# Kernel optimization log

Measured on AMD Instinct MI355X. Metric: run time of the kernel, lower is better.

The kernel has to match this reference:

```python
import jax, jax.numpy as jnp
import numpy as np

N_LAYER = 3
N_HEAD = 12
D_K = 64
D_V = 64
D_MODEL = 768
D_INNER = 4096
LN_EPS = 1e-5
BN_EPS = 1e-5
PAD_ID = 1


def _layernorm(x, g, b):
    m = jnp.mean(x, axis=-1, keepdims=True)
    v = jnp.mean((x - m) ** 2, axis=-1, keepdims=True)
    return g * (x - m) / jnp.sqrt(v + LN_EPS) + b


def _batchnorm(x, g, b):
    # training-mode BatchNorm1d: per-feature batch statistics
    m = jnp.mean(x, axis=0)
    v = jnp.mean((x - m) ** 2, axis=0)
    return g * (x - m) / jnp.sqrt(v + BN_EPS) + b


def setup_inputs() -> dict:
    key = jax.random.key(0)
    ks = jax.random.split(key, 24)
    B, C, S, H = 4, 4, 256, D_MODEL
    inp = {
        'input_ids': jax.random.randint(ks[0], (B, C, S), 0, 50000, dtype=jnp.int64) if jax.config.read('jax_enable_x64') else jax.random.randint(ks[0], (B, C, S), 0, 50000, dtype=jnp.int32),
        'roberta_attn': jax.random.normal(ks[1], (B, C, S, H), dtype=jnp.float32),
        'pooled_output': jax.random.normal(ks[2], (B * C, H), dtype=jnp.float32),
        'commonsense_mask': jax.random.uniform(ks[3], (B, C, S, S), dtype=jnp.float32),
        'dependency_mask': jax.random.uniform(ks[4], (B, C, S, S), dtype=jnp.float32),
        'entity_mask': jax.random.uniform(ks[5], (B, C, S), dtype=jnp.float32),
        'sentiment_mask': jax.random.uniform(ks[6], (B, C, S, S), dtype=jnp.float32),
    }
    s = 0.02
    inp['lin_w'] = s * jax.random.normal(ks[7], (H, N_LAYER * 4), dtype=jnp.float32)
    inp['lin_b'] = jnp.zeros((N_LAYER * 4,), jnp.float32)
    inp['Wq'] = s * jax.random.normal(ks[8], (N_LAYER, H, N_HEAD * D_K), dtype=jnp.float32)
    inp['bq'] = jnp.zeros((N_LAYER, N_HEAD * D_K), jnp.float32)
    inp['Wk'] = s * jax.random.normal(ks[9], (N_LAYER, H, N_HEAD * D_K), dtype=jnp.float32)
    inp['bk'] = jnp.zeros((N_LAYER, N_HEAD * D_K), jnp.float32)
    inp['Wv'] = s * jax.random.normal(ks[10], (N_LAYER, H, N_HEAD * D_V), dtype=jnp.float32)
    inp['bv'] = jnp.zeros((N_LAYER, N_HEAD * D_V), jnp.float32)
    inp['Wo'] = s * jax.random.normal(ks[11], (N_LAYER, N_HEAD * D_V, H), dtype=jnp.float32)
    inp['bo'] = jnp.zeros((N_LAYER, H), jnp.float32)
    inp['ln1_g'] = jnp.ones((N_LAYER, H), jnp.float32)
    inp['ln1_b'] = jnp.zeros((N_LAYER, H), jnp.float32)
    inp['W1'] = s * jax.random.normal(ks[12], (N_LAYER, H, D_INNER), dtype=jnp.float32)
    inp['b1'] = jnp.zeros((N_LAYER, D_INNER), jnp.float32)
    inp['W2'] = s * jax.random.normal(ks[13], (N_LAYER, D_INNER, H), dtype=jnp.float32)
    inp['b2'] = jnp.zeros((N_LAYER, H), jnp.float32)
    inp['ln2_g'] = jnp.ones((N_LAYER, H), jnp.float32)
    inp['ln2_b'] = jnp.zeros((N_LAYER, H), jnp.float32)
    inp['bnt_g'] = jnp.ones((H,), jnp.float32)
    inp['bnt_b'] = jnp.zeros((H,), jnp.float32)
    inp['pool_w'] = s * jax.random.normal(ks[14], (H, H), dtype=jnp.float32)
    inp['pool_b'] = jnp.zeros((H,), jnp.float32)
    inp['bn_g'] = jnp.ones((H,), jnp.float32)
    inp['bn_b'] = jnp.zeros((H,), jnp.float32)
    inp['cls_w'] = s * jax.random.normal(ks[15], (H, 1), dtype=jnp.float32)
    inp['cls_b'] = jnp.zeros((1,), jnp.float32)
    return inp


def reference(input_ids, roberta_attn, pooled_output, commonsense_mask, dependency_mask,
              entity_mask, sentiment_mask, lin_w, lin_b, Wq, bq, Wk, bk, Wv, bv, Wo, bo,
              ln1_g, ln1_b, W1, b1, W2, b2, ln2_g, ln2_b, bnt_g, bnt_b,
              pool_w, pool_b, bn_g, bn_b, cls_w, cls_b):
    B, C, S = input_ids.shape
    H = roberta_attn.shape[-1]
    N = B * C
    x = roberta_attn.reshape(N, S, H)

    # learned softmax fusion weights over the 4 relational masks, per layer
    w = jnp.mean(x, axis=1) @ lin_w + lin_b                       # [N, 3*4]
    w = jax.nn.softmax(w.reshape(N, N_LAYER, 4).transpose(1, 0, 2), axis=-1)  # [3, N, 4]

    ent = jnp.broadcast_to(entity_mask[:, :, None, :], (B, C, S, S))
    masks = jnp.stack([
        commonsense_mask.reshape(N, S, S),
        dependency_mask.reshape(N, S, S),
        ent.reshape(N, S, S),
        sentiment_mask.reshape(N, S, S),
    ], axis=1)                                                     # [N, 4, S, S]
    bias = jnp.einsum('lnm,nmqk->lnqk', w, masks)                  # [3, N, S, S]

    non_pad = (input_ids.reshape(N, S) != PAD_ID).astype(x.dtype)[:, :, None]  # [N, S, 1]

    enc = x
    scale = 1.0 / np.sqrt(D_K).astype(np.float32)
    for l in range(N_LAYER):
        residual = enc
        q = (enc @ Wq[l] + bq[l]).reshape(N, S, N_HEAD, D_K)
        k = (enc @ Wk[l] + bk[l]).reshape(N, S, N_HEAD, D_K)
        v = (enc @ Wv[l] + bv[l]).reshape(N, S, N_HEAD, D_V)
        scores = jnp.einsum('nqhd,nkhd->nhqk', q, k) * scale + bias[l][:, None]  # [N,H,S,S]
        attn = jax.nn.softmax(scores, axis=-1)
        o = jnp.einsum('nhqk,nkhd->nqhd', attn, v).reshape(N, S, N_HEAD * D_V)
        o = o @ Wo[l] + bo[l]
        enc = _layernorm(o + residual, ln1_g[l], ln1_b[l]) * non_pad
        residual = enc
        f = jax.nn.relu(enc @ W1[l] + b1[l]) @ W2[l] + b2[l]
        enc = _layernorm(f + residual, ln2_g[l], ln2_b[l]) * non_pad

    enc = _batchnorm(enc.reshape(N * S, H), bnt_g, bnt_b).reshape(N, S, H)
    seq = x + enc
    pooled = jnp.tanh(seq[:, 0] @ pool_w + pool_b)
    pooled = _batchnorm(pooled, bn_g, bn_b)
    logits = pooled @ cls_w + cls_b                                # [N, 1]
    return logits.reshape(-1, C)
```

## Files before the change

### kernel.cpp

```cpp
#include <hip/hip_runtime.h>
#include <hip/hip_bf16.h>
#include <math.h>

#define NSEQ 16
#define SEQ 256
#define H 768
#define NH 12
#define DKH 64
#define DI 4096
#define MROWS (NSEQ*SEQ)
#define QKVN (3*H)

typedef __bf16 v8bf __attribute__((ext_vector_type(8)));
typedef float  v4f  __attribute__((ext_vector_type(4)));
typedef short  v8s  __attribute__((ext_vector_type(8)));

__device__ inline unsigned short bf16b(float f) {
  __hip_bfloat16 h = __float2bfloat16(f);
  return *reinterpret_cast<unsigned short*>(&h);
}
__device__ inline float b2f(unsigned short b) {
  return __uint_as_float(((unsigned int)b) << 16);
}

__device__ __forceinline__ void gload16(const void* g, void* l) {
  __builtin_amdgcn_global_load_lds((const __attribute__((address_space(1))) void*)g,
                                   (__attribute__((address_space(3))) void*)l, 16, 0, 0);
}

enum { MODE_F32_BIAS=0, MODE_BF16_BIAS=1, MODE_BF16_BIAS_RELU=2, MODE_SCORES=3, MODE_PV=4 };

template<int BM, int BN, int MODE>
__global__ __launch_bounds__(256) void k_mm(
    const unsigned short* __restrict__ A, int lda, long long saN, long long saH,
    const unsigned short* __restrict__ B, int ldb, long long sbN, long long sbH,
    void* __restrict__ Cout, int ldc, long long scN, long long scH,
    const float* __restrict__ bias, int K, int nhdiv) {
  constexpr int MI = BM/32, NI = BN/32;
  constexpr int AISS = BM/32, BISS = BN/32;
  __shared__ unsigned short As[BM*64];
  __shared__ unsigned short Bs[BN*64];
  int t = threadIdx.x;
  int z = blockIdx.z, n = z / nhdiv, h = z - n*nhdiv;
  int lane = t & 63, wid = t >> 6, wr = wid >> 1, wc = wid & 1;

  const unsigned short* Ab = A + (size_t)n*saN + (size_t)h*saH + (size_t)blockIdx.y*BM*lda;
  const unsigned short* Bb = B + (size_t)n*sbN + (size_t)h*sbH + (size_t)blockIdx.x*BN*ldb;

  const unsigned short* aSrc[AISS];
  unsigned short* aDst[AISS];
#pragma unroll
  for (int r = 0; r < AISS; ++r) {
    int chunk = wid*AISS + r;
    int row = chunk*8 + (lane >> 3);
    int col = ((lane & 7) ^ (row & 7)) * 8;
    aSrc[r] = Ab + (size_t)row*lda + col;
    aDst[r] = &As[chunk*512];
  }
  const unsigned short* bSrc[BISS];
  unsigned short* bDst[BISS];
#pragma unroll
  for (int r = 0; r < BISS; ++r) {
    int chunk = wid*BISS + r;
    int row = chunk*8 + (lane >> 3);
    int col = ((lane & 7) ^ (row & 7)) * 8;
    bSrc[r] = Bb + (size_t)row*ldb + col;
    bDst[r] = &Bs[chunk*512];
  }

  v4f acc[MI][NI];
#pragma unroll
  for (int i = 0; i < MI; ++i)
#pragma unroll
    for (int j = 0; j < NI; ++j) acc[i][j] = (v4f){0.f,0.f,0.f,0.f};

  for (int k0 = 0; k0 < K; k0 += 64) {
#pragma unroll
    for (int r = 0; r < AISS; ++r) gload16(aSrc[r] + k0, aDst[r]);
#pragma unroll
    for (int r = 0; r < BISS; ++r) gload16(bSrc[r] + k0, bDst[r]);
    __syncthreads();
#pragma unroll
    for (int ks = 0; ks < 2; ++ks) {
      v8bf af[MI], bfr[NI];
#pragma unroll
      for (int i = 0; i < MI; ++i) {
        int row = wr*(BM/2) + i*16 + (lane & 15);
        int c = (ks*4 + (lane >> 4)) ^ (row & 7);
        af[i] = *(const v8bf*)&As[row*64 + c*8];
      }
#pragma unroll
      for (int j = 0; j < NI; ++j) {
        int row = wc*(BN/2) + j*16 + (lane & 15);
        int c = (ks*4 + (lane >> 4)) ^ (row & 7);
        bfr[j] = *(const v8bf*)&Bs[row*64 + c*8];
      }
#pragma unroll
      for (int i = 0; i < MI; ++i)
#pragma unroll
        for (int j = 0; j < NI; ++j)
          acc[i][j] = __builtin_amdgcn_mfma_f32_16x16x32_bf16(af[i], bfr[j], acc[i][j], 0, 0, 0);
    }
    __syncthreads();
  }

  float* Cf = (float*)Cout;
  unsigned short* Ch = (unsigned short*)Cout;
  size_t cb = (size_t)n*scN + (size_t)h*scH;
  int grow0 = blockIdx.y*BM + wr*(BM/2);
  int gcol0 = blockIdx.x*BN + wc*(BN/2);
#pragma unroll
  for (int i = 0; i < MI; ++i) {
#pragma unroll
    for (int j = 0; j < NI; ++j) {
      int col = gcol0 + j*16 + (lane & 15);
      float bval = 0.f;
      if (MODE == MODE_F32_BIAS || MODE == MODE_BF16_BIAS || MODE == MODE_BF16_BIAS_RELU)
        bval = bias[col];
#pragma unroll
      for (int r = 0; r < 4; ++r) {
        int row = grow0 + i*16 + (lane>>4)*4 + r;
        float v = acc[i][j][r];
        if (MODE == MODE_SCORES) {
          v = v*0.125f + bias[(size_t)n*65536 + (size_t)row*256 + col];
          Ch[cb + (size_t)row*ldc + col] = bf16b(v);
        } else if (MODE == MODE_F32_BIAS) {
          Cf[cb + (size_t)row*ldc + col] = v + bval;
        } else if (MODE == MODE_PV) {
          Ch[cb + (size_t)row*ldc + col] = bf16b(v);
        } else {
          v += bval;
          if (MODE == MODE_BF16_BIAS_RELU) v = fmaxf(v, 0.f);
          Ch[cb + (size_t)row*ldc + col] = bf16b(v);
        }
      }
    }
  }
}

__global__ __launch_bounds__(256) void k_wT(const float* __restrict__ in,
                                            unsigned short* __restrict__ out,
                                            int Nn, int Kk) {
  int n0 = blockIdx.x*64, k0 = blockIdx.y*64;
  __shared__ float T[64][72];
  int t = threadIdx.x;
  int r = t >> 4, c4 = (t & 15) * 4;
#pragma unroll
  for (int i = 0; i < 4; ++i) {
    float4 v = *(const float4*)(in + (size_t)(k0 + r + i*16)*Nn + n0 + c4);
    T[c4+0][r+i*16] = v.x; T[c4+1][r+i*16] = v.y;
    T[c4+2][r+i*16] = v.z; T[c4+3][r+i*16] = v.w;
  }
  __syncthreads();
  int c = t >> 3, r8 = (t & 7) * 8;
#pragma unroll
  for (int i = 0; i < 2; ++i) {
    int cc = c + i*32;
    v8s o;
#pragma unroll
    for (int j = 0; j < 8; ++j) o[j] = (short)bf16b(T[cc][r8+j]);
    *(v8s*)(out + (size_t)(n0+cc)*Kk + k0 + r8) = o;
  }
}

__global__ void k_bqkv(const float* __restrict__ bq, const float* __restrict__ bk,
                       const float* __restrict__ bv, float* __restrict__ o) {
  int i = blockIdx.x*256 + threadIdx.x;
  if (i >= 3*QKVN) return;
  int l = i / QKVN, j = i - l*QKVN;
  float v = (j < H) ? bq[l*H + j] : (j < 2*H) ? bk[l*H + j - H] : bv[l*H + j - 2*H];
  o[i] = v;
}

__global__ __launch_bounds__(256) void k_cast(const float* __restrict__ x,
                                              float* __restrict__ enc,
                                              unsigned short* __restrict__ enc16) {
  size_t i = ((size_t)blockIdx.x*256 + threadIdx.x)*4;
  float4 v = *(const float4*)(x + i);
  *(float4*)(enc + i) = v;
  ushort4 u = { bf16b(v.x), bf16b(v.y), bf16b(v.z), bf16b(v.w) };
  *(ushort4*)(enc16 + i) = u;
}

__global__ __launch_bounds__(256) void k_vT(const unsigned short* __restrict__ qkv,
                                            unsigned short* __restrict__ vT) {
  int z = blockIdx.x, n = z/NH, h = z - n*NH;
  const unsigned short* src = qkv + (size_t)n*SEQ*QKVN + 2*H + (size_t)h*DKH;
  __shared__ unsigned short tile[64][264];
  int t = threadIdx.x;
  int r0 = t >> 3, d0 = (t & 7) * 8;
#pragma unroll
  for (int i = 0; i < 8; ++i) {
    int r = r0 + i*32;
    v8s vv = *(const v8s*)(src + (size_t)r*QKVN + d0);
#pragma unroll
    for (int j = 0; j < 8; ++j) tile[d0+j][r] = (unsigned short)vv[j];
  }
  __syncthreads();
  int d = t >> 2, rb = (t & 3) * 64;
  unsigned short* dst = vT + (size_t)z*DKH*SEQ + (size_t)d*SEQ + rb;
#pragma unroll
  for (int i = 0; i < 8; ++i)
    *(v8s*)(dst + i*8) = *(const v8s*)&tile[d][rb + i*8];
}

__global__ __launch_bounds__(256) void k_fusion_weights(
    const float* __restrict__ x, const float* __restrict__ lin_w,
    const float* __restrict__ lin_b, float* __restrict__ wsoft) {
  int n = blockIdx.x, t = threadIdx.x;
  __shared__ float xm[H];
  __shared__ float sred[4];
  __shared__ float logits[12];
  if (t < 192) {
    const float4* p = (const float4*)(x + (size_t)n*SEQ*H) + t;
    float4 s = {0.f,0.f,0.f,0.f};
    for (int r = 0; r < SEQ; ++r) {
      float4 v = p[(size_t)r*192];
      s.x += v.x; s.y += v.y; s.z += v.z; s.w += v.w;
    }
    xm[t*4+0] = s.x*(1.0f/SEQ); xm[t*4+1] = s.y*(1.0f/SEQ);
    xm[t*4+2] = s.z*(1.0f/SEQ); xm[t*4+3] = s.w*(1.0f/SEQ);
  }
  __syncthreads();
  float lacc[12];
#pragma unroll
  for (int j = 0; j < 12; ++j) lacc[j] = 0.f;
  for (int hh = t; hh < H; hh += 256) {
    float xv = xm[hh];
#pragma unroll
    for (int j = 0; j < 12; ++j) lacc[j] += xv * lin_w[hh*12 + j];
  }
  for (int j = 0; j < 12; ++j) {
    float v = lacc[j];
#pragma unroll
    for (int m = 1; m < 64; m <<= 1) v += __shfl_xor(v, m, 64);
    if ((t & 63) == 0) sred[t >> 6] = v;
    __syncthreads();
    if (t == 0) logits[j] = sred[0]+sred[1]+sred[2]+sred[3] + lin_b[j];
    __syncthreads();
  }
  if (t < 3) {
    int l = t;
    float mx = -1e30f;
    for (int m = 0; m < 4; ++m) mx = fmaxf(mx, logits[l*4+m]);
    float e[4], s = 0.f;
    for (int m = 0; m < 4; ++m) { e[m] = expf(logits[l*4+m]-mx); s += e[m]; }
    for (int m = 0; m < 4; ++m) wsoft[(l*NSEQ + n)*4 + m] = e[m]/s;
  }
}

__global__ __launch_bounds__(256) void k_bias(
    const float* __restrict__ cm, const float* __restrict__ dm,
    const float* __restrict__ ent, const float* __restrict__ sm,
    const float* __restrict__ wsoft, int l, float* __restrict__ bias) {
  int g = blockIdx.x*256 + threadIdx.x;
  int n = g >> 14;
  int k4 = g & 63;
  const float* w = wsoft + (l*NSEQ + n)*4;
  float w0 = w[0], w1 = w[1], w2 = w[2], w3 = w[3];
  float4 c = ((const float4*)cm)[g];
  float4 d = ((const float4*)dm)[g];
  float4 s = ((const float4*)sm)[g];
  float4 e = ((const float4*)(ent + (size_t)n*SEQ))[k4];
  float4 o;
  o.x = w0*c.x + w1*d.x + w2*e.x + w3*s.x;
  o.y = w0*c.y + w1*d.y + w2*e.y + w3*s.y;
  o.z = w0*c.z + w1*d.z + w2*e.z + w3*s.z;
  o.w = w0*c.w + w1*d.w + w2*e.w + w3*s.w;
  ((float4*)bias)[g] = o;
}

__global__ void k_nonpad(const int* __restrict__ ids, float* __restrict__ npad) {
  int i = blockIdx.x*256 + threadIdx.x;
  if (i < MROWS) npad[i] = (ids[i] != 1) ? 1.0f : 0.0f;
}

__global__ __launch_bounds__(256) void k_softmax16(const unsigned short* __restrict__ s,
                                                   unsigned short* __restrict__ p) {
  int row = blockIdx.x*4 + (threadIdx.x >> 6);
  int lane = threadIdx.x & 63;
  ushort4 u = *(const ushort4*)(s + (size_t)row*SEQ + lane*4);
  float v0 = b2f(u.x), v1 = b2f(u.y), v2 = b2f(u.z), v3 = b2f(u.w);
  float mx = fmaxf(fmaxf(v0, v1), fmaxf(v2, v3));
#pragma unroll
  for (int m = 1; m < 64; m <<= 1) mx = fmaxf(mx, __shfl_xor(mx, m, 64));
  v0 = expf(v0-mx); v1 = expf(v1-mx); v2 = expf(v2-mx); v3 = expf(v3-mx);
  float sum = v0+v1+v2+v3;
#pragma unroll
  for (int m = 1; m < 64; m <<= 1) sum += __shfl_xor(sum, m, 64);
  float r = 1.0f/sum;
  ushort4 o = { bf16b(v0*r), bf16b(v1*r), bf16b(v2*r), bf16b(v3*r) };
  *(ushort4*)(p + (size_t)row*SEQ + lane*4) = o;
}

__global__ __launch_bounds__(256) void k_ln(
    const float* __restrict__ f, float* __restrict__ enc,
    unsigned short* __restrict__ enc16,
    const float* __restrict__ g, const float* __restrict__ b,
    const float* __restrict__ npad) {
  int r = blockIdx.x, t = threadIdx.x;
  size_t base = (size_t)r*H;
  float v0 = f[base+t]     + enc[base+t];
  float v1 = f[base+t+256] + enc[base+t+256];
  float v2 = f[base+t+512] + enc[base+t+512];
  __shared__ float sred[4];
  float s = v0+v1+v2;
#pragma unroll
  for (int m = 1; m < 64; m <<= 1) s += __shfl_xor(s, m, 64);
  if ((t & 63) == 0) sred[t >> 6] = s;
  __syncthreads();
  float mean = (sred[0]+sred[1]+sred[2]+sred[3]) * (1.0f/H);
  __syncthreads();
  float d0 = v0-mean, d1 = v1-mean, d2 = v2-mean;
  float ss = d0*d0 + d1*d1 + d2*d2;
#pragma unroll
  for (int m = 1; m < 64; m <<= 1) ss += __shfl_xor(ss, m, 64);
  if ((t & 63) == 0) sred[t >> 6] = ss;
  __syncthreads();
  float var = (sred[0]+sred[1]+sred[2]+sred[3]) * (1.0f/H);
  float rstd = 1.0f/sqrtf(var + 1e-5f);
  float npv = npad[r];
  float o0 = (g[t]    *d0*rstd + b[t]    )*npv;
  float o1 = (g[t+256]*d1*rstd + b[t+256])*npv;
  float o2 = (g[t+512]*d2*rstd + b[t+512])*npv;
  enc[base+t]     = o0; enc[base+t+256] = o1; enc[base+t+512] = o2;
  enc16[base+t]     = bf16b(o0);
  enc16[base+t+256] = bf16b(o1);
  enc16[base+t+512] = bf16b(o2);
}

__global__ __launch_bounds__(256) void k_colstats(
    const float* __restrict__ enc, float* __restrict__ csum, float* __restrict__ csq) {
  int r0 = blockIdx.x*64, t = threadIdx.x;
  float s0=0,s1=0,s2=0,q0=0,q1=0,q2=0;
  for (int r = 0; r < 64; ++r) {
    const float* row = enc + (size_t)(r0+r)*H;
    float a = row[t], b = row[t+256], c = row[t+512];
    s0 += a; s1 += b; s2 += c;
    q0 += a*a; q1 += b*b; q2 += c*c;
  }
  atomicAdd(&csum[t],     s0); atomicAdd(&csum[t+256], s1); atomicAdd(&csum[t+512], s2);
  atomicAdd(&csq[t],      q0); atomicAdd(&csq[t+256],  q1); atomicAdd(&csq[t+512],  q2);
}

__global__ __launch_bounds__(256) void k_poolprep(
    const float* __restrict__ x, const float* __restrict__ enc,
    const float* __restrict__ csum, const float* __restrict__ csq,
    const float* __restrict__ bnt_g, const float* __restrict__ bnt_b,
    float* __restrict__ ps0) {
  int n = blockIdx.x, t = threadIdx.x;
  for (int hh = t; hh < H; hh += 256) {
    float m = csum[hh] * (1.0f/MROWS);
    float var = csq[hh] * (1.0f/MROWS) - m*m;
    float rstd = 1.0f/sqrtf(var + 1e-5f);
    float e = enc[(size_t)n*SEQ*H + hh];
    ps0[n*H + hh] = x[(size_t)n*SEQ*H + hh] + bnt_g[hh]*(e-m)*rstd + bnt_b[hh];
  }
}

__global__ __launch_bounds__(256) void k_poolmm(
    const float* __restrict__ ps0, const float* __restrict__ pool_w,
    const float* __restrict__ pool_b, float* __restrict__ pooled) {
  int n = blockIdx.y, jb = blockIdx.x*64;
  __shared__ float s0[H];
  __shared__ float part[4][64];
  int t = threadIdx.x;
  for (int hh = t; hh < H; hh += 256) s0[hh] = ps0[n*H + hh];
  __syncthreads();
  int j = t & 63, q = t >> 6;
  float a = 0.f;
  int h0 = q*192;
  for (int hh = h0; hh < h0+192; ++hh)
    a = fmaf(s0[hh], pool_w[(size_t)hh*H + jb + j], a);
  part[q][j] = a;
  __syncthreads();
  if (t < 64) {
    float v = part[0][t]+part[1][t]+part[2][t]+part[3][t] + pool_b[jb+t];
    pooled[n*H + jb + t] = tanhf(v);
  }
}

__global__ __launch_bounds__(256) void k_final(
    const float* __restrict__ pooled, const float* __restrict__ bn_g,
    const float* __restrict__ bn_b, const float* __restrict__ cls_w,
    const float* __restrict__ cls_b, float* __restrict__ out) {
  int t = threadIdx.x;
  float acc[16];
#pragma unroll
  for (int n = 0; n < 16; ++n) acc[n] = 0.f;
  for (int hh = t; hh < H; hh += 256) {
    float p[16]; float m = 0.f;
#pragma unroll
    for (int n = 0; n < 16; ++n) { p[n] = pooled[n*H + hh]; m += p[n]; }
    m *= (1.0f/16.f);
    float var = 0.f;
#pragma unroll
    for (int n = 0; n < 16; ++n) { float d = p[n]-m; var += d*d; }
    var *= (1.0f/16.f);
    float rstd = 1.0f/sqrtf(var + 1e-5f);
    float gw = bn_g[hh]*rstd*cls_w[hh];
    float off = bn_b[hh]*cls_w[hh];
#pragma unroll
    for (int n = 0; n < 16; ++n) acc[n] += (p[n]-m)*gw + off;
  }
  __shared__ float sred[4];
  for (int n = 0; n < 16; ++n) {
    float v = acc[n];
#pragma unroll
    for (int m = 1; m < 64; m <<= 1) v += __shfl_xor(v, m, 64);
    if ((t & 63) == 0) sred[t >> 6] = v;
    __syncthreads();
    if (t == 0) out[n] = sred[0]+sred[1]+sred[2]+sred[3] + cls_b[0];
    __syncthreads();
  }
}

extern "C" void kernel_launch(void* const* d_in, const int* in_sizes, int n_in,
                              void* d_out, int out_size, void* d_ws, size_t ws_size,
                              hipStream_t stream) {
  const int*   input_ids = (const int*)  d_in[0];
  const float* x       = (const float*)d_in[1];
  const float* cm      = (const float*)d_in[3];
  const float* dm      = (const float*)d_in[4];
  const float* ent     = (const float*)d_in[5];
  const float* sm      = (const float*)d_in[6];
  const float* lin_w   = (const float*)d_in[7];
  const float* lin_b   = (const float*)d_in[8];
  const float* Wq      = (const float*)d_in[9];
  const float* bq      = (const float*)d_in[10];
  const float* Wk      = (const float*)d_in[11];
  const float* bk      = (const float*)d_in[12];
  const float* Wv      = (const float*)d_in[13];
  const float* bv      = (const float*)d_in[14];
  const float* Wo      = (const float*)d_in[15];
  const float* bo      = (const float*)d_in[16];
  const float* ln1_g   = (const float*)d_in[17];
  const float* ln1_b   = (const float*)d_in[18];
  const float* W1      = (const float*)d_in[19];
  const float* b1      = (const float*)d_in[20];
  const float* W2      = (const float*)d_in[21];
  const float* b2      = (const float*)d_in[22];
  const float* ln2_g   = (const float*)d_in[23];
  const float* ln2_b   = (const float*)d_in[24];
  const float* bnt_g   = (const float*)d_in[25];
  const float* bnt_b   = (const float*)d_in[26];
  const float* pool_w  = (const float*)d_in[27];
  const float* pool_b  = (const float*)d_in[28];
  const float* bn_g    = (const float*)d_in[29];
  const float* bn_b    = (const float*)d_in[30];
  const float* cls_w   = (const float*)d_in[31];
  const float* cls_b   = (const float*)d_in[32];
  float* out = (float*)d_out;
  (void)ws_size; (void)n_in; (void)in_sizes; (void)out_size;

  char* wsb = (char*)d_ws;
  size_t off = 0;
  auto alloc = [&](size_t bytes) {
    void* p = (void*)(wsb + off);
    off += (bytes + 255) & ~(size_t)255;
    return p;
  };
  float* enc            = (float*)alloc((size_t)MROWS*H*4);
  unsigned short* enc16 = (unsigned short*)alloc((size_t)MROWS*H*2);
  unsigned short* qkv16 = (unsigned short*)alloc((size_t)MROWS*QKVN*2);
  unsigned short* vT    = (unsigned short*)alloc((size_t)192*DKH*SEQ*2);
  unsigned short* ob16  = (unsigned short*)alloc((size_t)MROWS*H*2);
  float* fbuf           = (float*)alloc((size_t)MROWS*H*4);
  unsigned short* scoresB = (unsigned short*)alloc((size_t)MROWS*DI*2);
  unsigned short* hidden16 = scoresB;
  unsigned short* P16   = (unsigned short*)alloc((size_t)192*SEQ*SEQ*2);
  float* biasb          = (float*)alloc((size_t)NSEQ*SEQ*SEQ*4);
  unsigned short* WqkvT = (unsigned short*)alloc((size_t)3*QKVN*H*2);
  unsigned short* WoT   = (unsigned short*)alloc((size_t)3*H*H*2);
  unsigned short* W1T   = (unsigned short*)alloc((size_t)3*DI*H*2);
  unsigned short* W2T   = (unsigned short*)alloc((size_t)3*H*DI*2);
  float* bqkv   = (float*)alloc(3*QKVN*4);
  float* wsoft  = (float*)alloc(3*16*4*4);
  float* npad   = (float*)alloc(MROWS*4);
  float* csum   = (float*)alloc(H*4);
  float* csq    = (float*)alloc(H*4);
  float* ps0    = (float*)alloc(16*H*4);
  float* pooled = (float*)alloc(16*H*4);

  k_cast<<<MROWS*H/1024, 256, 0, stream>>>(x, enc, enc16);
  k_fusion_weights<<<16, 256, 0, stream>>>(x, lin_w, lin_b, wsoft);
  k_nonpad<<<MROWS/256, 256, 0, stream>>>(input_ids, npad);
  k_bqkv<<<27, 256, 0, stream>>>(bq, bk, bv, bqkv);
  for (int l = 0; l < 3; ++l) {
    k_wT<<<dim3(12,12), 256, 0, stream>>>(Wq + (size_t)l*H*H, WqkvT + (size_t)l*QKVN*H,           H, H);
    k_wT<<<dim3(12,12), 256, 0, stream>>>(Wk + (size_t)l*H*H, WqkvT + (size_t)l*QKVN*H + H*H,     H, H);
    k_wT<<<dim3(12,12), 256, 0, stream>>>(Wv + (size_t)l*H*H, WqkvT + (size_t)l*QKVN*H + 2*H*H,   H, H);
    k_wT<<<dim3(12,12), 256, 0, stream>>>(Wo + (size_t)l*H*H, WoT + (size_t)l*H*H,                H, H);
    k_wT<<<dim3(64,12), 256, 0, stream>>>(W1 + (size_t)l*H*DI, W1T + (size_t)l*DI*H,              DI, H);
    k_wT<<<dim3(12,64), 256, 0, stream>>>(W2 + (size_t)l*DI*H, W2T + (size_t)l*H*DI,              H, DI);
  }

  for (int l = 0; l < 3; ++l) {
    k_bias<<<1024, 256, 0, stream>>>(cm, dm, ent, sm, wsoft, l, biasb);
    k_mm<128,128,MODE_BF16_BIAS><<<dim3(18,32,1), 256, 0, stream>>>(
        enc16, H, 0, 0, WqkvT + (size_t)l*QKVN*H, H, 0, 0,
        qkv16, QKVN, 0, 0, bqkv + l*QKVN, H, 1);
    k_mm<64,64,MODE_SCORES><<<dim3(4,4,192), 256, 0, stream>>>(
        qkv16, QKVN, (long long)SEQ*QKVN, DKH,
        qkv16 + H, QKVN, (long long)SEQ*QKVN, DKH,
        scoresB, SEQ, (long long)NH*SEQ*SEQ, (long long)SEQ*SEQ,
        biasb, DKH, NH);
    k_softmax16<<<192*SEQ/4, 256, 0, stream>>>(scoresB, P16);
    k_vT<<<192, 256, 0, stream>>>(qkv16, vT);
    k_mm<64,64,MODE_PV><<<dim3(1,4,192), 256, 0, stream>>>(
        P16, SEQ, (long long)NH*SEQ*SEQ, (long long)SEQ*SEQ,
        vT, SEQ, (long long)NH*DKH*SEQ, (long long)DKH*SEQ,
        ob16, H, (long long)SEQ*H, DKH,
        nullptr, SEQ, NH);
    k_mm<128,64,MODE_F32_BIAS><<<dim3(12,32,1), 256, 0, stream>>>(
        ob16, H, 0, 0, WoT + (size_t)l*H*H, H, 0, 0,
        fbuf, H, 0, 0, bo + l*H, H, 1);
    k_ln<<<MROWS, 256, 0, stream>>>(fbuf, enc, enc16, ln1_g + l*H, ln1_b + l*H, npad);
    k_mm<128,128,MODE_BF16_BIAS_RELU><<<dim3(32,32,1), 256, 0, stream>>>(
        enc16, H, 0, 0, W1T + (size_t)l*DI*H, H, 0, 0,
        hidden16, DI, 0, 0, b1 + l*DI, H, 1);
    k_mm<128,64,MODE_F32_BIAS><<<dim3(12,32,1), 256, 0, stream>>>(
        hidden16, DI, 0, 0, W2T + (size_t)l*H*DI, DI, 0, 0,
        fbuf, H, 0, 0, b2 + l*H, DI, 1);
    k_ln<<<MROWS, 256, 0, stream>>>(fbuf, enc, enc16, ln2_g + l*H, ln2_b + l*H, npad);
  }

  hipMemsetAsync(csum, 0, H*sizeof(float), stream);
  hipMemsetAsync(csq,  0, H*sizeof(float), stream);
  k_colstats<<<64, 256, 0, stream>>>(enc, csum, csq);
  k_poolprep<<<16, 256, 0, stream>>>(x, enc, csum, csq, bnt_g, bnt_b, ps0);
  k_poolmm<<<dim3(12,16), 256, 0, stream>>>(ps0, pool_w, pool_b, pooled);
  k_final<<<1, 256, 0, stream>>>(pooled, bn_g, bn_b, cls_w, cls_b, out);
}
```

Baseline: 763.6 us.

## Double-buffer LDS loads in GEMM, add XCD block swizzle, retile output projections

Adds a double-buffered LDS path to the GEMM kernel, so the next K tile's global-to-LDS loads are issued before computing the current tile, with explicit vmcnt waits and barriers. Adds an XCD-aware remapping of block indices meant to improve L2 locality across the eight dies. Switches the Wo and W2 GEMMs from 128x64 to 64x64 tiles (doubling block count) and enables double buffering for them and for the PV product. The hardcoded vmcnt(4) assumes exactly four outstanding loads per thread, which ties the DB path to 64x64 tiles. Smaller tiles also lower data reuse per block.

```diff
diff --git a/kernel.cpp b/kernel.cpp
--- a/kernel.cpp
+++ b/kernel.cpp
@@ -30,7 +30,7 @@
 
 enum { MODE_F32_BIAS=0, MODE_BF16_BIAS=1, MODE_BF16_BIAS_RELU=2, MODE_SCORES=3, MODE_PV=4 };
 
-template<int BM, int BN, int MODE>
+template<int BM, int BN, int MODE, bool DB, bool SWZ>
 __global__ __launch_bounds__(256) void k_mm(
     const unsigned short* __restrict__ A, int lda, long long saN, long long saH,
     const unsigned short* __restrict__ B, int ldb, long long sbN, long long sbH,
@@ -38,34 +38,45 @@
     const float* __restrict__ bias, int K, int nhdiv) {
   constexpr int MI = BM/32, NI = BN/32;
   constexpr int AISS = BM/32, BISS = BN/32;
-  __shared__ unsigned short As[BM*64];
-  __shared__ unsigned short Bs[BN*64];
+  constexpr int TA = BM*64, TB = BN*64;
+  static_assert(!DB || (BM==64 && BN==64), "DB path assumes vmcnt(4)");
+  __shared__ unsigned short As[(DB?2:1)*TA];
+  __shared__ unsigned short Bs[(DB?2:1)*TB];
   int t = threadIdx.x;
   int z = blockIdx.z, n = z / nhdiv, h = z - n*nhdiv;
   int lane = t & 63, wid = t >> 6, wr = wid >> 1, wc = wid & 1;
 
-  const unsigned short* Ab = A + (size_t)n*saN + (size_t)h*saH + (size_t)blockIdx.y*BM*lda;
-  const unsigned short* Bb = B + (size_t)n*sbN + (size_t)h*sbH + (size_t)blockIdx.x*BN*ldb;
-
-  const unsigned short* aSrc[AISS];
-  unsigned short* aDst[AISS];
+  int bx = blockIdx.x, by = blockIdx.y;
+  if (SWZ) {
+    int gx = gridDim.x;
+    int nwg = gx * gridDim.y;
+    int lin = by*gx + bx;
+    int q = nwg >> 3, r = nwg & 7;
+    int xcd = lin & 7, idx = lin >> 3;
+    int swz = (xcd < r) ? (xcd*(q+1) + idx) : (r*(q+1) + (xcd-r)*q + idx);
+    bx = swz % gx; by = swz / gx;
+  }
+
+  const unsigned short* Ab = A + (size_t)n*saN + (size_t)h*saH + (size_t)by*BM*lda;
+  const unsigned short* Bb = B + (size_t)n*sbN + (size_t)h*sbH + (size_t)bx*BN*ldb;
+
+  const unsigned short* aSrc[AISS]; int aOff[AISS];
 #pragma unroll
   for (int r = 0; r < AISS; ++r) {
     int chunk = wid*AISS + r;
     int row = chunk*8 + (lane >> 3);
     int col = ((lane & 7) ^ (row & 7)) * 8;
     aSrc[r] = Ab + (size_t)row*lda + col;
-    aDst[r] = &As[chunk*512];
-  }
-  const unsigned short* bSrc[BISS];
-  unsigned short* bDst[BISS];
+    aOff[r] = chunk*512;
+  }
+  const unsigned short* bSrc[BISS]; int bOff[BISS];
 #pragma unroll
   for (int r = 0; r < BISS; ++r) {
     int chunk = wid*BISS + r;
     int row = chunk*8 + (lane >> 3);
     int col = ((lane & 7) ^ (row & 7)) * 8;
     bSrc[r] = Bb + (size_t)row*ldb + col;
-    bDst[r] = &Bs[chunk*512];
+    bOff[r] = chunk*512;
   }
 
   v4f acc[MI][NI];
@@ -74,41 +85,89 @@
 #pragma unroll
     for (int j = 0; j < NI; ++j) acc[i][j] = (v4f){0.f,0.f,0.f,0.f};
 
-  for (int k0 = 0; k0 < K; k0 += 64) {
-#pragma unroll
-    for (int r = 0; r < AISS; ++r) gload16(aSrc[r] + k0, aDst[r]);
-#pragma unroll
-    for (int r = 0; r < BISS; ++r) gload16(bSrc[r] + k0, bDst[r]);
-    __syncthreads();
-#pragma unroll
-    for (int ks = 0; ks < 2; ++ks) {
-      v8bf af[MI], bfr[NI];
-#pragma unroll
-      for (int i = 0; i < MI; ++i) {
-        int row = wr*(BM/2) + i*16 + (lane & 15);
-        int c = (ks*4 + (lane >> 4)) ^ (row & 7);
-        af[i] = *(const v8bf*)&As[row*64 + c*8];
+  if (DB) {
+    int nt = K >> 6;
+#pragma unroll
+    for (int r = 0; r < AISS; ++r) gload16(aSrc[r], &As[aOff[r]]);
+#pragma unroll
+    for (int r = 0; r < BISS; ++r) gload16(bSrc[r], &Bs[bOff[r]]);
+    int cur = 0;
+    for (int tt = 0; tt < nt; ++tt) {
+      if (tt + 1 < nt) {
+        int k1 = (tt+1) << 6, nb = (cur^1);
+#pragma unroll
+        for (int r = 0; r < AISS; ++r) gload16(aSrc[r] + k1, &As[nb*TA + aOff[r]]);
+#pragma unroll
+        for (int r = 0; r < BISS; ++r) gload16(bSrc[r] + k1, &Bs[nb*TB + bOff[r]]);
+        asm volatile("s_waitcnt vmcnt(4)" ::: "memory");
+      } else {
+        asm volatile("s_waitcnt vmcnt(0)" ::: "memory");
       }
-#pragma unroll
-      for (int j = 0; j < NI; ++j) {
-        int row = wc*(BN/2) + j*16 + (lane & 15);
-        int c = (ks*4 + (lane >> 4)) ^ (row & 7);
-        bfr[j] = *(const v8bf*)&Bs[row*64 + c*8];
+      __builtin_amdgcn_s_barrier();
+      asm volatile("" ::: "memory");
+#pragma unroll
+      for (int ks = 0; ks < 2; ++ks) {
+        v8bf af[MI], bfr[NI];
+#pragma unroll
+        for (int i = 0; i < MI; ++i) {
+          int row = wr*(BM/2) + i*16 + (lane & 15);
+          int c = (ks*4 + (lane >> 4)) ^ (row & 7);
+          af[i] = *(const v8bf*)&As[cur*TA + row*64 + c*8];
+        }
+#pragma unroll
+        for (int j = 0; j < NI; ++j) {
+          int row = wc*(BN/2) + j*16 + (lane & 15);
+          int c = (ks*4 + (lane >> 4)) ^ (row & 7);
+          bfr[j] = *(const v8bf*)&Bs[cur*TB + row*64 + c*8];
+        }
+#pragma unroll
+        for (int i = 0; i < MI; ++i)
+#pragma unroll
+          for (int j = 0; j < NI; ++j)
+            acc[i][j] = __builtin_amdgcn_mfma_f32_16x16x32_bf16(af[i], bfr[j], acc[i][j], 0, 0, 0);
       }
-#pragma unroll
-      for (int i = 0; i < MI; ++i)
-#pragma unroll
-        for (int j = 0; j < NI; ++j)
-          acc[i][j] = __builtin_amdgcn_mfma_f32_16x16x32_bf16(af[i], bfr[j], acc[i][j], 0, 0, 0);
+      asm volatile("s_waitcnt lgkmcnt(0)" ::: "memory");
+      __builtin_amdgcn_s_barrier();
+      asm volatile("" ::: "memory");
+      cur ^= 1;
     }
-    __syncthreads();
+  } else {
+    for (int k0 = 0; k0 < K; k0 += 64) {
+#pragma unroll
+      for (int r = 0; r < AISS; ++r) gload16(aSrc[r] + k0, &As[aOff[r]]);
+#pragma unroll
+      for (int r = 0; r < BISS; ++r) gload16(bSrc[r] + k0, &Bs[bOff[r]]);
+      __syncthreads();
+#pragma unroll
+      for (int ks = 0; ks < 2; ++ks) {
+        v8bf af[MI], bfr[NI];
+#pragma unroll
+        for (int i = 0; i < MI; ++i) {
+          int row = wr*(BM/2) + i*16 + (lane & 15);
+          int c = (ks*4 + (lane >> 4)) ^ (row & 7);
+          af[i] = *(const v8bf*)&As[row*64 + c*8];
+        }
+#pragma unroll
+        for (int j = 0; j < NI; ++j) {
+          int row = wc*(BN/2) + j*16 + (lane & 15);
+          int c = (ks*4 + (lane >> 4)) ^ (row & 7);
+          bfr[j] = *(const v8bf*)&Bs[row*64 + c*8];
+        }
+#pragma unroll
+        for (int i = 0; i < MI; ++i)
+#pragma unroll
+          for (int j = 0; j < NI; ++j)
+            acc[i][j] = __builtin_amdgcn_mfma_f32_16x16x32_bf16(af[i], bfr[j], acc[i][j], 0, 0, 0);
+      }
+      __syncthreads();
+    }
   }
 
   float* Cf = (float*)Cout;
   unsigned short* Ch = (unsigned short*)Cout;
   size_t cb = (size_t)n*scN + (size_t)h*scH;
-  int grow0 = blockIdx.y*BM + wr*(BM/2);
-  int gcol0 = blockIdx.x*BN + wc*(BN/2);
+  int grow0 = by*BM + wr*(BM/2);
+  int gcol0 = bx*BN + wc*(BN/2);
 #pragma unroll
   for (int i = 0; i < MI; ++i) {
 #pragma unroll
@@ -497,29 +556,29 @@
 
   for (int l = 0; l < 3; ++l) {
     k_bias<<<1024, 256, 0, stream>>>(cm, dm, ent, sm, wsoft, l, biasb);
-    k_mm<128,128,MODE_BF16_BIAS><<<dim3(18,32,1), 256, 0, stream>>>(
+    k_mm<128,128,MODE_BF16_BIAS,false,true><<<dim3(18,32,1), 256, 0, stream>>>(
         enc16, H, 0, 0, WqkvT + (size_t)l*QKVN*H, H, 0, 0,
         qkv16, QKVN, 0, 0, bqkv + l*QKVN, H, 1);
-    k_mm<64,64,MODE_SCORES><<<dim3(4,4,192), 256, 0, stream>>>(
+    k_mm<64,64,MODE_SCORES,false,false><<<dim3(4,4,192), 256, 0, stream>>>(
         qkv16, QKVN, (long long)SEQ*QKVN, DKH,
         qkv16 + H, QKVN, (long long)SEQ*QKVN, DKH,
         scoresB, SEQ, (long long)NH*SEQ*SEQ, (long long)SEQ*SEQ,
         biasb, DKH, NH);
     k_softmax16<<<192*SEQ/4, 256, 0, stream>>>(scoresB, P16);
     k_vT<<<192, 256, 0, stream>>>(qkv16, vT);
-    k_mm<64,64,MODE_PV><<<dim3(1,4,192), 256, 0, stream>>>(
+    k_mm<64,64,MODE_PV,true,false><<<dim3(1,4,192), 256, 0, stream>>>(
         P16, SEQ, (long long)NH*SEQ*SEQ, (long long)SEQ*SEQ,
         vT, SEQ, (long long)NH*DKH*SEQ, (long long)DKH*SEQ,
         ob16, H, (long long)SEQ*H, DKH,
         nullptr, SEQ, NH);
-    k_mm<128,64,MODE_F32_BIAS><<<dim3(12,32,1), 256, 0, stream>>>(
+    k_mm<64,64,MODE_F32_BIAS,true,true><<<dim3(12,64,1), 256, 0, stream>>>(
         ob16, H, 0, 0, WoT + (size_t)l*H*H, H, 0, 0,
         fbuf, H, 0, 0, bo + l*H, H, 1);
     k_ln<<<MROWS, 256, 0, stream>>>(fbuf, enc, enc16, ln1_g + l*H, ln1_b + l*H, npad);
-    k_mm<128,128,MODE_BF16_BIAS_RELU><<<dim3(32,32,1), 256, 0, stream>>>(
+    k_mm<128,128,MODE_BF16_BIAS_RELU,false,true><<<dim3(32,32,1), 256, 0, stream>>>(
         enc16, H, 0, 0, W1T + (size_t)l*DI*H, H, 0, 0,
         hidden16, DI, 0, 0, b1 + l*DI, H, 1);
-    k_mm<128,64,MODE_F32_BIAS><<<dim3(12,32,1), 256, 0, stream>>>(
+    k_mm<64,64,MODE_F32_BIAS,true,true><<<dim3(12,64,1), 256, 0, stream>>>(
         hidden16, DI, 0, 0, W2T + (size_t)l*H*DI, DI, 0, 0,
         fbuf, H, 0, 0, b2 + l*H, DI, 1);
     k_ln<<<MROWS, 256, 0, stream>>>(fbuf, enc, enc16, ln2_g + l*H, ln2_b + l*H, npad);
```

Measured after the change: 719.5 us. 5.8% less time.
